# Optimization experiments

Measured on AMD Instinct MI355X. Metric: run time of the kernel, lower is better.

The kernel has to match this reference:

```python
import jax, jax.numpy as jnp
import numpy as np

K = -1.0          # manifold curvature (hyperbolic / Poincare ball)
EPS = 1e-15

def _artanh(x):
    return jnp.arctanh(jnp.clip(x, -1.0 + 1e-7, 1.0 - 1e-7))

def _norm(x, keepdims=True):
    return jnp.sqrt(jnp.maximum(jnp.sum(x * x, axis=-1, keepdims=keepdims), EPS * EPS))

def expmap0(u):
    # sqrt(-K) == 1 for K = -1
    un = _norm(u)
    return jnp.tanh(un) * u / un

def logmap0(x):
    xn = _norm(x)
    return _artanh(xn) * x / xn

def mobius_matvec(m, x):
    xn = _norm(x)
    mx = x @ m
    mxn = _norm(mx)
    return jnp.tanh(mxn / xn * _artanh(xn)) * mx / mxn

def mobius_scalar_mul(r, x):
    xn = _norm(x)
    return jnp.tanh(r * _artanh(xn)) * x / xn

def mobius_add(x, y):
    x2 = jnp.sum(x * x, -1, keepdims=True)
    y2 = jnp.sum(y * y, -1, keepdims=True)
    xy = jnp.sum(x * y, -1, keepdims=True)
    num = (1.0 - 2.0 * K * xy - K * y2) * x + (1.0 + K * x2) * y
    den = 1.0 - 2.0 * K * xy + K * K * x2 * y2
    return num / jnp.maximum(den, EPS)

def lambda_x(x, keepdims=True):
    x2 = jnp.sum(x * x, -1, keepdims=keepdims)
    return 2.0 / jnp.maximum(1.0 + K * x2, EPS)

def kappa_layer(X, A, W):
    # mobius matvec + adjacency-weighted gyromidpoint (lincomb=True) + sigma
    XW = mobius_matvec(W, X)                       # [N, D]
    gamma = lambda_x(XW)                           # [N, 1] conformal factor
    denom = A @ (gamma - 1.0)                      # [N, 1]
    nom = A @ (gamma * XW)                         # [N, D]
    denom = jnp.where(denom >= 0, jnp.maximum(denom, 1e-10), jnp.minimum(denom, -1e-10))
    a_mean = mobius_scalar_mul(0.5, nom / denom)   # gyromidpoint
    alpha = jnp.sum(A, axis=1, keepdims=True)      # lincomb scaling
    AXW = mobius_scalar_mul(alpha, a_mean)
    return expmap0(jax.nn.relu(logmap0(AXW)))      # sigma = exp(relu(log(x)))

def get_logits(X, W, b):
    z = mobius_add(-b[None, :, :], X[:, None, :])              # [N, C, D]
    zn = jnp.maximum(_norm(z, keepdims=False), 1e-10)          # [N, C]
    an = jnp.maximum(jnp.linalg.norm(W, axis=0), 1e-10)        # [C]
    za = jnp.einsum('ncd,dc->nc', z, W)                        # [N, C]
    dist = jnp.arcsinh(2.0 * za / ((1.0 + K * zn ** 2) * an))  # arsin_k, kappa*|kappa| = -1
    lam_b = lambda_x(b, keepdims=False)                        # [C]
    return (lam_b * an) * dist

def _forward(X, A_hat, W1, W2, W_logits, p_ks):
    X = kappa_layer(X, A_hat, W1)
    X = kappa_layer(X, A_hat, W2)
    logits = get_logits(X, W_logits, p_ks)
    return A_hat @ logits                          # aggregate_logits=True


def setup_inputs() -> dict:
    key = jax.random.key(0)
    ks = jax.random.split(key, 6)
    N, D, C = 8192, 32, 16
    # node features are points on the manifold: expmap0 of small tangent vectors
    X = expmap0(jax.random.normal(ks[0], (N, D), jnp.float32) * 0.1)
    # dense non-negative normalized-adjacency-like weights, row sums ~ 1.5
    A_hat = jax.random.uniform(ks[1], (N, N), dtype=jnp.float32) * (3.0 / N)
    W1 = jax.random.normal(ks[2], (D, D), jnp.float32) * 0.01
    W2 = jax.random.normal(ks[3], (D, D), jnp.float32) * 0.01
    W_logits = jax.random.normal(ks[4], (D, C), jnp.float32) * 0.01
    p_ks = expmap0(jax.random.normal(ks[5], (C, D), jnp.float32) * 0.01)
    return {"X": X, "A_hat": A_hat, "W1": W1, "W2": W2,
            "W_logits": W_logits, "p_ks": p_ks}


def reference(X, A_hat, W1, W2, W_logits, p_ks):
    return _forward(X, A_hat, W1, W2, W_logits, p_ks)
```

## Files before the change

kernel.cpp:

```cpp
#include <hip/hip_runtime.h>

#define N_NODES 8192
#define DIM 32
#define NCLS 16
#define NCOLC 36
#define NKT (N_NODES / 32)
#define RT_STRIDE ((size_t)NKT * 512)
#define PITCH 520
#define KSEG 512

typedef __bf16 bf16x8 __attribute__((ext_vector_type(8)));
typedef float f32x4 __attribute__((ext_vector_type(4)));

__device__ inline unsigned short f2bf(float f) {
  unsigned u = __float_as_uint(f);
  u = u + 0x7FFFu + ((u >> 16) & 1u);
  return (unsigned short)(u >> 16);
}

__device__ inline float artanh_pos(float x) {
  x = fminf(x, 1.0f - 1e-7f);
  return 0.5f * logf((1.0f + x) / (1.0f - x));
}

__device__ inline size_t g_tile_idx(int c, int n) {
  return ((size_t)(n >> 5) * 3 + (c >> 4)) * 512 + (size_t)((c & 15) * 32 + (n & 31));
}
__device__ inline size_t l_tile_idx(int c, int n) {
  return (size_t)(n >> 5) * 512 + (size_t)(c * 32 + (n & 31));
}

__global__ __launch_bounds__(256) void k_mmc(const float* __restrict__ A,
                                             const unsigned short* __restrict__ GT,
                                             unsigned short* __restrict__ Abf,
                                             float* __restrict__ Cpart) {
  __shared__ __align__(16) unsigned short buf0[16 * PITCH];
  __shared__ __align__(16) unsigned short buf1[16 * PITCH];
  float* lds_r = (float*)buf0;
  const int t = threadIdx.x;
  const int rt = blockIdx.x >> 3;
  const int q = blockIdx.x & 7;
  const int ks0 = 2 * q, ks1 = 2 * q + 1;
  const int lane = t & 63;
  const int w = t >> 6;
  const int lr = lane & 15;
  const int lkg = lane >> 4;
  const int vrow = t >> 7;
  const int vk = (t & 127) * 4;
  const int poff = lr * 32 + lkg * 8;

  const float* srcbase = A + (size_t)(rt * 16) * N_NODES;

  f32x4 r0[8];
#pragma unroll
  for (int v = 0; v < 8; v++)
    r0[v] = __builtin_nontemporal_load(
        (const f32x4*)(srcbase + (size_t)(2 * v + vrow) * N_NODES + ks0 * KSEG + vk));
#pragma unroll
  for (int v = 0; v < 8; v++) {
    uint2 o;
    o.x = f2bf(r0[v][0]) | ((unsigned)f2bf(r0[v][1]) << 16);
    o.y = f2bf(r0[v][2]) | ((unsigned)f2bf(r0[v][3]) << 16);
    *(uint2*)(buf0 + (2 * v + vrow) * PITCH + vk) = o;
  }
  __syncthreads();

  f32x4 r1[8];
#pragma unroll
  for (int v = 0; v < 8; v++)
    r1[v] = __builtin_nontemporal_load(
        (const f32x4*)(srcbase + (size_t)(2 * v + vrow) * N_NODES + ks1 * KSEG + vk));

  f32x4 acc[3];
#pragma unroll
  for (int nf = 0; nf < 3; nf++) acc[nf] = (f32x4){0.f, 0.f, 0.f, 0.f};
#pragma unroll
  for (int i = 0; i < 4; i++) {
    const int kt2 = 4 * w + i;
    bf16x8 a = *(const bf16x8*)(buf0 + lr * PITCH + kt2 * 32 + lkg * 8);
#pragma unroll
    for (int nf = 0; nf < 3; nf++) {
      bf16x8 b = *(const bf16x8*)(GT + ((size_t)(ks0 * 16 + kt2) * 3 + nf) * 512 + poff);
      acc[nf] = __builtin_amdgcn_mfma_f32_16x16x32_bf16(a, b, acc[nf], 0, 0, 0);
    }
  }
  {
    unsigned short* dst = Abf + (size_t)(rt * 16 + ks0) * 8192;
#pragma unroll
    for (int u = 0; u < 4; u++) {
      const int p = u * 256 + t;
      const int kt = p >> 6;
      const int qq = p & 63;
      bf16x8 val = *(const bf16x8*)(buf0 + (qq >> 2) * PITCH + kt * 32 + (qq & 3) * 8);
      *(bf16x8*)(dst + (size_t)p * 8) = val;
    }
  }

#pragma unroll
  for (int v = 0; v < 8; v++) {
    uint2 o;
    o.x = f2bf(r1[v][0]) | ((unsigned)f2bf(r1[v][1]) << 16);
    o.y = f2bf(r1[v][2]) | ((unsigned)f2bf(r1[v][3]) << 16);
    *(uint2*)(buf1 + (2 * v + vrow) * PITCH + vk) = o;
  }
  __syncthreads();

#pragma unroll
  for (int i = 0; i < 4; i++) {
    const int kt2 = 4 * w + i;
    bf16x8 a = *(const bf16x8*)(buf1 + lr * PITCH + kt2 * 32 + lkg * 8);
#pragma unroll
    for (int nf = 0; nf < 3; nf++) {
      bf16x8 b = *(const bf16x8*)(GT + ((size_t)(ks1 * 16 + kt2) * 3 + nf) * 512 + poff);
      acc[nf] = __builtin_amdgcn_mfma_f32_16x16x32_bf16(a, b, acc[nf], 0, 0, 0);
    }
  }
  {
    unsigned short* dst = Abf + (size_t)(rt * 16 + ks1) * 8192;
#pragma unroll
    for (int u = 0; u < 4; u++) {
      const int p = u * 256 + t;
      const int kt = p >> 6;
      const int qq = p & 63;
      bf16x8 val = *(const bf16x8*)(buf1 + (qq >> 2) * PITCH + kt * 32 + (qq & 3) * 8);
      *(bf16x8*)(dst + (size_t)p * 8) = val;
    }
  }
  __syncthreads();

#pragma unroll
  for (int nf = 0; nf < 3; nf++)
#pragma unroll
    for (int j = 0; j < 4; j++)
      lds_r[(w * 16 + lkg * 4 + j) * 48 + nf * 16 + lr] = acc[nf][j];
  __syncthreads();
  for (int e = t; e < 16 * 36; e += 256) {
    const int row = e / 36;
    const int col = e % 36;
    float s = lds_r[row * 48 + col] + lds_r[768 + row * 48 + col] +
              lds_r[1536 + row * 48 + col] + lds_r[2304 + row * 48 + col];
    Cpart[((size_t)q * N_NODES + rt * 16 + row) * NCOLC + col] = s;
  }
}

__device__ inline void pre_math(const float* __restrict__ Wl, const float x[DIM],
                                unsigned short* __restrict__ GT, int n) {
  float xn2 = 0.f;
#pragma unroll
  for (int i = 0; i < DIM; i++) xn2 += x[i] * x[i];
  float xn = sqrtf(fmaxf(xn2, 1e-30f));
  float mx[DIM];
#pragma unroll
  for (int j = 0; j < DIM; j++) mx[j] = 0.f;
  for (int i = 0; i < DIM; i++) {
    float xi = x[i];
#pragma unroll
    for (int j = 0; j < DIM; j++) mx[j] = fmaf(xi, Wl[i * DIM + j], mx[j]);
  }
  float mxn2 = 0.f;
#pragma unroll
  for (int j = 0; j < DIM; j++) mxn2 += mx[j] * mx[j];
  float mxn = sqrtf(fmaxf(mxn2, 1e-30f));
  float t = tanhf(mxn / xn * artanh_pos(xn));
  float sc = t / mxn;
  float xw[DIM];
  float x2n = 0.f;
#pragma unroll
  for (int j = 0; j < DIM; j++) { xw[j] = sc * mx[j]; x2n += xw[j] * xw[j]; }
  float gamma = 2.0f / fmaxf(1.0f - x2n, 1e-15f);
#pragma unroll
  for (int c = 0; c < DIM; c++) GT[g_tile_idx(c, n)] = f2bf(gamma * xw[c]);
  GT[g_tile_idx(32, n)] = f2bf(gamma - 1.0f);
  GT[g_tile_idx(33, n)] = f2bf(1.0f);
#pragma unroll
  for (int c = DIM + 2; c < 48; c++) GT[g_tile_idx(c, n)] = 0;
}

__global__ void k_pre1(const float* __restrict__ X, const float* __restrict__ W,
                       unsigned short* __restrict__ GT) {
  __shared__ float Wl[DIM * DIM];
  for (int i = threadIdx.x; i < DIM * DIM; i += blockDim.x) Wl[i] = W[i];
  __syncthreads();
  const int n = blockIdx.x * blockDim.x + threadIdx.x;
  float x[DIM];
#pragma unroll
  for (int i = 0; i < DIM; i += 4) {
    float4 v = *(const float4*)(X + (size_t)n * DIM + i);
    x[i] = v.x; x[i + 1] = v.y; x[i + 2] = v.z; x[i + 3] = v.w;
  }
  pre_math(Wl, x, GT, n);
}

template <int SPLITS>
__device__ inline void post_math(const float* __restrict__ Cpart, int n, float xo[DIM]) {
  float acc[NCOLC];
#pragma unroll
  for (int c = 0; c < NCOLC; c++) acc[c] = 0.f;
  for (int s = 0; s < SPLITS; s++) {
    const float4* p = (const float4*)(Cpart + ((size_t)s * N_NODES + n) * NCOLC);
#pragma unroll
    for (int qq = 0; qq < NCOLC / 4; qq++) {
      float4 v = p[qq];
      acc[qq * 4 + 0] += v.x; acc[qq * 4 + 1] += v.y;
      acc[qq * 4 + 2] += v.z; acc[qq * 4 + 3] += v.w;
    }
  }
  float denom = acc[32];
  float alpha = acc[33];
  denom = (denom >= 0.f) ? fmaxf(denom, 1e-10f) : fminf(denom, -1e-10f);
  float inv = 1.0f / denom;
  float v[DIM];
  float vn2 = 0.f;
#pragma unroll
  for (int c = 0; c < DIM; c++) { v[c] = acc[c] * inv; vn2 += v[c] * v[c]; }
  float vn = sqrtf(fmaxf(vn2, 1e-30f));
  float un = alpha * 0.5f * artanh_pos(vn);
  float su = un / vn;
  float r[DIM];
  float rn2 = 0.f;
#pragma unroll
  for (int c = 0; c < DIM; c++) { r[c] = fmaxf(su * v[c], 0.f); rn2 += r[c] * r[c]; }
  float rn = sqrtf(fmaxf(rn2, 1e-30f));
  float so = tanhf(rn) / rn;
#pragma unroll
  for (int c = 0; c < DIM; c++) xo[c] = so * r[c];
}

__global__ void k_postpre(const float* __restrict__ Cpart, const float* __restrict__ W,
                          unsigned short* __restrict__ GT) {
  __shared__ float Wl[DIM * DIM];
  for (int i = threadIdx.x; i < DIM * DIM; i += blockDim.x) Wl[i] = W[i];
  __syncthreads();
  const int n = blockIdx.x * blockDim.x + threadIdx.x;
  float x[DIM];
  post_math<8>(Cpart, n, x);
  pre_math(Wl, x, GT, n);
}

__global__ void k_postlogits(const float* __restrict__ Cpart, const float* __restrict__ Wl_g,
                             const float* __restrict__ B_g, unsigned short* __restrict__ LT) {
  __shared__ float Wc[DIM * NCLS];
  __shared__ float Bc[NCLS * DIM];
  __shared__ float an_s[NCLS], lam_s[NCLS], b2_s[NCLS];
  for (int i = threadIdx.x; i < DIM * NCLS; i += blockDim.x) { Wc[i] = Wl_g[i]; Bc[i] = B_g[i]; }
  __syncthreads();
  if (threadIdx.x < NCLS) {
    int c = threadIdx.x;
    float b2 = 0.f, w2 = 0.f;
    for (int d = 0; d < DIM; d++) {
      b2 += Bc[c * DIM + d] * Bc[c * DIM + d];
      w2 += Wc[d * NCLS + c] * Wc[d * NCLS + c];
    }
    b2_s[c] = b2;
    an_s[c] = fmaxf(sqrtf(w2), 1e-10f);
    lam_s[c] = 2.0f / fmaxf(1.0f - b2, 1e-15f);
  }
  __syncthreads();
  const int n = blockIdx.x * blockDim.x + threadIdx.x;
  float x[DIM];
  post_math<16>(Cpart, n, x);
  float y2 = 0.f;
#pragma unroll
  for (int i = 0; i < DIM; i++) y2 += x[i] * x[i];
  for (int c = 0; c < NCLS; c++) {
    float b2 = b2_s[c];
    float bx = 0.f;
    for (int d = 0; d < DIM; d++) bx += Bc[c * DIM + d] * x[d];
    float xy = -bx;
    float f1 = 1.0f + 2.0f * xy + y2;
    float f2 = 1.0f - b2;
    float den = fmaxf(1.0f + 2.0f * xy + b2 * y2, 1e-15f);
    float invden = 1.0f / den;
    float zn2 = 0.f, za = 0.f;
    for (int d = 0; d < DIM; d++) {
      float z = (f1 * (-Bc[c * DIM + d]) + f2 * x[d]) * invden;
      zn2 += z * z;
      za += z * Wc[d * NCLS + c];
    }
    float zn = fmaxf(sqrtf(fmaxf(zn2, 1e-30f)), 1e-10f);
    float dist = asinhf(2.0f * za / ((1.0f - zn * zn) * an_s[c]));
    LT[l_tile_idx(c, n)] = f2bf(lam_s[c] * an_s[c] * dist);
  }
}

template <int NF>
__global__ __launch_bounds__(256) void k_mm(const unsigned short* __restrict__ A,
                                            const unsigned short* __restrict__ BT,
                                            float* __restrict__ Cpart) {
  const int lane = threadIdx.x & 63;
  const int wid = threadIdx.x >> 6;
  const int r0 = blockIdx.x * 128 + wid * 32;
  const int kt0 = blockIdx.y * (512 / 32);
  const int lr = lane & 15;
  const int lkg = lane >> 4;
  const int poff = lr * 32 + lkg * 8;
  const int BS = (NF == 3) ? 3 : 1;
  f32x4 acc[2][NF];
#pragma unroll
  for (int m = 0; m < 2; m++)
#pragma unroll
    for (int nf = 0; nf < NF; nf++) acc[m][nf] = (f32x4){0.f, 0.f, 0.f, 0.f};
  const unsigned short* pa0 = A + ((size_t)(r0 >> 4) * NKT + kt0) * 512 + poff;
  const unsigned short* pa1 = pa0 + RT_STRIDE;
  const unsigned short* pbB = BT + (size_t)kt0 * BS * 512 + poff;
#pragma unroll 4
  for (int kt = 0; kt < 16; kt++) {
    bf16x8 a0 = *(const bf16x8*)(pa0 + (size_t)kt * 512);
    bf16x8 a1 = *(const bf16x8*)(pa1 + (size_t)kt * 512);
#pragma unroll
    for (int nf = 0; nf < NF; nf++) {
      bf16x8 b = *(const bf16x8*)(pbB + (size_t)(kt * BS + nf) * 512);
      acc[0][nf] = __builtin_amdgcn_mfma_f32_16x16x32_bf16(a0, b, acc[0][nf], 0, 0, 0);
      acc[1][nf] = __builtin_amdgcn_mfma_f32_16x16x32_bf16(a1, b, acc[1][nf], 0, 0, 0);
    }
  }
  const int NCOL = (NF == 3) ? NCOLC : NF * 16;
  float* Cb = Cpart + (size_t)blockIdx.y * N_NODES * NCOL;
#pragma unroll
  for (int m = 0; m < 2; m++)
#pragma unroll
    for (int nf = 0; nf < NF; nf++) {
      if (NF == 3 && nf == 2 && lr >= 4) continue;
#pragma unroll
      for (int j = 0; j < 4; j++) {
        int row = r0 + m * 16 + lkg * 4 + j;
        int col = nf * 16 + lr;
        Cb[(size_t)row * NCOL + col] = acc[m][nf][j];
      }
    }
}

template <int TOTAL, int SPLITS>
__global__ void k_red(const float* __restrict__ part, float* __restrict__ outb) {
  int i = blockIdx.x * blockDim.x + threadIdx.x;
  if (i < TOTAL) {
    float s = 0.f;
#pragma unroll
    for (int qq = 0; qq < SPLITS; qq++) s += part[(size_t)qq * TOTAL + i];
    outb[i] = s;
  }
}

extern "C" void kernel_launch(void* const* d_in, const int* in_sizes, int n_in,
                              void* d_out, int out_size, void* d_ws, size_t ws_size,
                              hipStream_t stream) {
  (void)in_sizes; (void)n_in; (void)out_size; (void)ws_size;
  const float* X  = (const float*)d_in[0];
  const float* A  = (const float*)d_in[1];
  const float* W1 = (const float*)d_in[2];
  const float* W2 = (const float*)d_in[3];
  const float* WL = (const float*)d_in[4];
  const float* PK = (const float*)d_in[5];
  float* out = (float*)d_out;

  char* ws = (char*)d_ws;
  unsigned short* Abf = (unsigned short*)ws;
  unsigned short* GT  = (unsigned short*)(ws + 134217728);
  float* Cpart        = (float*)(ws + 135004160);
  unsigned short* LT  = (unsigned short*)(ws + 153878528);

  k_pre1<<<N_NODES / 64, 64, 0, stream>>>(X, W1, GT);
  k_mmc<<<4096, 256, 0, stream>>>(A, GT, Abf, Cpart);
  k_postpre<<<N_NODES / 64, 64, 0, stream>>>(Cpart, W2, GT);

  k_mm<3><<<dim3(64, 16), 256, 0, stream>>>(Abf, GT, Cpart);
  k_postlogits<<<N_NODES / 64, 64, 0, stream>>>(Cpart, WL, PK, LT);

  k_mm<1><<<dim3(64, 16), 256, 0, stream>>>(Abf, LT, Cpart);
  k_red<N_NODES * NCLS, 16><<<(N_NODES * NCLS + 255) / 256, 256, 0, stream>>>(Cpart, out);
}
```

Before: 181.3 us.

## Parallelize split reductions across 256 threads, halve k_mm splits, nontemporal A stores

The post kernels now launch 256 threads per 64 nodes, so four sub-groups each sum two partial splits and the results are combined through shared memory before the per-node math runs on one wavefront. k_mm now uses 8 K-splits of 32 tiles each instead of 16 of 16, which halves the partial-sum traffic and the work in the reduction kernels. The bf16 copy of A is written with nontemporal stores to avoid polluting the cache. The risks are lower k_mm parallelism (512 blocks), idle threads during the post tail, and a fixed SPLITS=8 that k_postlogits and k_red must stay consistent with.

```diff
diff --git a/kernel.cpp b/kernel.cpp
--- a/kernel.cpp
+++ b/kernel.cpp
@@ -8,6 +8,7 @@
 #define RT_STRIDE ((size_t)NKT * 512)
 #define PITCH 520
 #define KSEG 512
+#define SPLITS 8
 
 typedef __bf16 bf16x8 __attribute__((ext_vector_type(8)));
 typedef float f32x4 __attribute__((ext_vector_type(4)));
@@ -92,7 +93,7 @@
       const int kt = p >> 6;
       const int qq = p & 63;
       bf16x8 val = *(const bf16x8*)(buf0 + (qq >> 2) * PITCH + kt * 32 + (qq & 3) * 8);
-      *(bf16x8*)(dst + (size_t)p * 8) = val;
+      __builtin_nontemporal_store(val, (bf16x8*)(dst + (size_t)p * 8));
     }
   }
 
@@ -123,7 +124,7 @@
       const int kt = p >> 6;
       const int qq = p & 63;
       bf16x8 val = *(const bf16x8*)(buf1 + (qq >> 2) * PITCH + kt * 32 + (qq & 3) * 8);
-      *(bf16x8*)(dst + (size_t)p * 8) = val;
+      __builtin_nontemporal_store(val, (bf16x8*)(dst + (size_t)p * 8));
     }
   }
   __syncthreads();
@@ -191,12 +192,14 @@
   pre_math(Wl, x, GT, n);
 }
 
-template <int SPLITS>
-__device__ inline void post_math(const float* __restrict__ Cpart, int n, float xo[DIM]) {
+__device__ inline void par_reduce(const float* __restrict__ Cpart, int n, int sub, int nl,
+                                  float red[4][64][NCOLC]) {
   float acc[NCOLC];
 #pragma unroll
   for (int c = 0; c < NCOLC; c++) acc[c] = 0.f;
-  for (int s = 0; s < SPLITS; s++) {
+#pragma unroll
+  for (int si = 0; si < 2; si++) {
+    const int s = sub * 2 + si;
     const float4* p = (const float4*)(Cpart + ((size_t)s * N_NODES + n) * NCOLC);
 #pragma unroll
     for (int qq = 0; qq < NCOLC / 4; qq++) {
@@ -205,6 +208,11 @@
       acc[qq * 4 + 2] += v.z; acc[qq * 4 + 3] += v.w;
     }
   }
+#pragma unroll
+  for (int c = 0; c < NCOLC; c++) red[sub][nl][c] = acc[c];
+}
+
+__device__ inline void post_tail(const float acc[NCOLC], float xo[DIM]) {
   float denom = acc[32];
   float alpha = acc[33];
   denom = (denom >= 0.f) ? fmaxf(denom, 1e-10f) : fminf(denom, -1e-10f);
@@ -226,26 +234,44 @@
   for (int c = 0; c < DIM; c++) xo[c] = so * r[c];
 }
 
-__global__ void k_postpre(const float* __restrict__ Cpart, const float* __restrict__ W,
-                          unsigned short* __restrict__ GT) {
+__global__ __launch_bounds__(256) void k_postpre(const float* __restrict__ Cpart,
+                                                 const float* __restrict__ W,
+                                                 unsigned short* __restrict__ GT) {
   __shared__ float Wl[DIM * DIM];
-  for (int i = threadIdx.x; i < DIM * DIM; i += blockDim.x) Wl[i] = W[i];
-  __syncthreads();
-  const int n = blockIdx.x * blockDim.x + threadIdx.x;
-  float x[DIM];
-  post_math<8>(Cpart, n, x);
-  pre_math(Wl, x, GT, n);
-}
-
-__global__ void k_postlogits(const float* __restrict__ Cpart, const float* __restrict__ Wl_g,
-                             const float* __restrict__ B_g, unsigned short* __restrict__ LT) {
+  __shared__ float red[4][64][NCOLC];
+  const int t = threadIdx.x;
+  const int nl = t & 63;
+  const int sub = t >> 6;
+  for (int i = t; i < DIM * DIM; i += 256) Wl[i] = W[i];
+  const int n = blockIdx.x * 64 + nl;
+  par_reduce(Cpart, n, sub, nl, red);
+  __syncthreads();
+  if (sub == 0) {
+    float acc[NCOLC];
+#pragma unroll
+    for (int c = 0; c < NCOLC; c++)
+      acc[c] = ((red[0][nl][c] + red[1][nl][c]) + red[2][nl][c]) + red[3][nl][c];
+    float x[DIM];
+    post_tail(acc, x);
+    pre_math(Wl, x, GT, n);
+  }
+}
+
+__global__ __launch_bounds__(256) void k_postlogits(const float* __restrict__ Cpart,
+                                                    const float* __restrict__ Wl_g,
+                                                    const float* __restrict__ B_g,
+                                                    unsigned short* __restrict__ LT) {
   __shared__ float Wc[DIM * NCLS];
   __shared__ float Bc[NCLS * DIM];
   __shared__ float an_s[NCLS], lam_s[NCLS], b2_s[NCLS];
-  for (int i = threadIdx.x; i < DIM * NCLS; i += blockDim.x) { Wc[i] = Wl_g[i]; Bc[i] = B_g[i]; }
-  __syncthreads();
-  if (threadIdx.x < NCLS) {
-    int c = threadIdx.x;
+  __shared__ float red[4][64][NCOLC];
+  const int t = threadIdx.x;
+  const int nl = t & 63;
+  const int sub = t >> 6;
+  for (int i = t; i < DIM * NCLS; i += 256) { Wc[i] = Wl_g[i]; Bc[i] = B_g[i]; }
+  __syncthreads();
+  if (t < NCLS) {
+    int c = t;
     float b2 = 0.f, w2 = 0.f;
     for (int d = 0; d < DIM; d++) {
       b2 += Bc[c * DIM + d] * Bc[c * DIM + d];
@@ -255,31 +281,38 @@
     an_s[c] = fmaxf(sqrtf(w2), 1e-10f);
     lam_s[c] = 2.0f / fmaxf(1.0f - b2, 1e-15f);
   }
-  __syncthreads();
-  const int n = blockIdx.x * blockDim.x + threadIdx.x;
-  float x[DIM];
-  post_math<16>(Cpart, n, x);
-  float y2 = 0.f;
-#pragma unroll
-  for (int i = 0; i < DIM; i++) y2 += x[i] * x[i];
-  for (int c = 0; c < NCLS; c++) {
-    float b2 = b2_s[c];
-    float bx = 0.f;
-    for (int d = 0; d < DIM; d++) bx += Bc[c * DIM + d] * x[d];
-    float xy = -bx;
-    float f1 = 1.0f + 2.0f * xy + y2;
-    float f2 = 1.0f - b2;
-    float den = fmaxf(1.0f + 2.0f * xy + b2 * y2, 1e-15f);
-    float invden = 1.0f / den;
-    float zn2 = 0.f, za = 0.f;
-    for (int d = 0; d < DIM; d++) {
-      float z = (f1 * (-Bc[c * DIM + d]) + f2 * x[d]) * invden;
-      zn2 += z * z;
-      za += z * Wc[d * NCLS + c];
-    }
-    float zn = fmaxf(sqrtf(fmaxf(zn2, 1e-30f)), 1e-10f);
-    float dist = asinhf(2.0f * za / ((1.0f - zn * zn) * an_s[c]));
-    LT[l_tile_idx(c, n)] = f2bf(lam_s[c] * an_s[c] * dist);
+  const int n = blockIdx.x * 64 + nl;
+  par_reduce(Cpart, n, sub, nl, red);
+  __syncthreads();
+  if (sub == 0) {
+    float acc[NCOLC];
+#pragma unroll
+    for (int c = 0; c < NCOLC; c++)
+      acc[c] = ((red[0][nl][c] + red[1][nl][c]) + red[2][nl][c]) + red[3][nl][c];
+    float x[DIM];
+    post_tail(acc, x);
+    float y2 = 0.f;
+#pragma unroll
+    for (int i = 0; i < DIM; i++) y2 += x[i] * x[i];
+    for (int c = 0; c < NCLS; c++) {
+      float b2 = b2_s[c];
+      float bx = 0.f;
+      for (int d = 0; d < DIM; d++) bx += Bc[c * DIM + d] * x[d];
+      float xy = -bx;
+      float f1 = 1.0f + 2.0f * xy + y2;
+      float f2 = 1.0f - b2;
+      float den = fmaxf(1.0f + 2.0f * xy + b2 * y2, 1e-15f);
+      float invden = 1.0f / den;
+      float zn2 = 0.f, za = 0.f;
+      for (int d = 0; d < DIM; d++) {
+        float z = (f1 * (-Bc[c * DIM + d]) + f2 * x[d]) * invden;
+        zn2 += z * z;
+        za += z * Wc[d * NCLS + c];
+      }
+      float zn = fmaxf(sqrtf(fmaxf(zn2, 1e-30f)), 1e-10f);
+      float dist = asinhf(2.0f * za / ((1.0f - zn * zn) * an_s[c]));
+      LT[l_tile_idx(c, n)] = f2bf(lam_s[c] * an_s[c] * dist);
+    }
   }
 }
 
@@ -290,7 +323,7 @@
   const int lane = threadIdx.x & 63;
   const int wid = threadIdx.x >> 6;
   const int r0 = blockIdx.x * 128 + wid * 32;
-  const int kt0 = blockIdx.y * (512 / 32);
+  const int kt0 = blockIdx.y * 32;
   const int lr = lane & 15;
   const int lkg = lane >> 4;
   const int poff = lr * 32 + lkg * 8;
@@ -304,7 +337,7 @@
   const unsigned short* pa1 = pa0 + RT_STRIDE;
   const unsigned short* pbB = BT + (size_t)kt0 * BS * 512 + poff;
 #pragma unroll 4
-  for (int kt = 0; kt < 16; kt++) {
+  for (int kt = 0; kt < 32; kt++) {
     bf16x8 a0 = *(const bf16x8*)(pa0 + (size_t)kt * 512);
     bf16x8 a1 = *(const bf16x8*)(pa1 + (size_t)kt * 512);
 #pragma unroll
@@ -330,7 +363,7 @@
     }
 }
 
-template <int TOTAL, int SPLITS>
+template <int TOTAL>
 __global__ void k_red(const float* __restrict__ part, float* __restrict__ outb) {
   int i = blockIdx.x * blockDim.x + threadIdx.x;
   if (i < TOTAL) {
@@ -361,11 +394,11 @@
 
   k_pre1<<<N_NODES / 64, 64, 0, stream>>>(X, W1, GT);
   k_mmc<<<4096, 256, 0, stream>>>(A, GT, Abf, Cpart);
-  k_postpre<<<N_NODES / 64, 64, 0, stream>>>(Cpart, W2, GT);
-
-  k_mm<3><<<dim3(64, 16), 256, 0, stream>>>(Abf, GT, Cpart);
-  k_postlogits<<<N_NODES / 64, 64, 0, stream>>>(Cpart, WL, PK, LT);
-
-  k_mm<1><<<dim3(64, 16), 256, 0, stream>>>(Abf, LT, Cpart);
-  k_red<N_NODES * NCLS, 16><<<(N_NODES * NCLS + 255) / 256, 256, 0, stream>>>(Cpart, out);
-}
+  k_postpre<<<N_NODES / 64, 256, 0, stream>>>(Cpart, W2, GT);
+
+  k_mm<3><<<dim3(64, 8), 256, 0, stream>>>(Abf, GT, Cpart);
+  k_postlogits<<<N_NODES / 64, 256, 0, stream>>>(Cpart, WL, PK, LT);
+
+  k_mm<1><<<dim3(64, 8), 256, 0, stream>>>(Abf, LT, Cpart);
+  k_red<N_NODES * NCLS><<<(N_NODES * NCLS + 255) / 256, 256, 0, stream>>>(Cpart, out);
+}
```

Result: faster. 175.9 us (-3.0%).
